# Performance work log

Hardware: AMD Instinct MI355X
Metric: run time of the kernel (lower is better)

## Reference

```python
import jax, jax.numpy as jnp
import numpy as np

INPUT_SIZE = 512
HIDDEN_SIZE = 256
B, S = 8, 2048


def setup_inputs() -> dict:
    key = jax.random.key(0)
    ks = jax.random.split(key, 9)
    d = INPUT_SIZE
    q = jax.random.normal(ks[0], (B, S, 2 * HIDDEN_SIZE), dtype=jnp.float32)
    k = jax.random.normal(ks[1], (B, S, d), dtype=jnp.float32)
    v = jax.random.normal(ks[2], (B, S, d), dtype=jnp.float32)
    # Params: module uses nn.init.normal_ (std=1); keep normal but scale for stability.
    Wq = jax.random.normal(ks[3], (2 * HIDDEN_SIZE, d), dtype=jnp.float32) * 0.02
    bq = jax.random.normal(ks[4], (d,), dtype=jnp.float32) * 0.02
    Wk = jax.random.normal(ks[5], (d, d), dtype=jnp.float32) * 0.02
    bk = jax.random.normal(ks[6], (d,), dtype=jnp.float32) * 0.02
    Wv = jax.random.normal(ks[7], (d, d), dtype=jnp.float32) * 0.02
    bv = jax.random.normal(ks[8], (d,), dtype=jnp.float32) * 0.02
    return {"q": q, "k": k, "v": v, "Wq": Wq, "bq": bq, "Wk": Wk, "bk": bk, "Wv": Wv, "bv": bv}


def reference(q, k, v, Wq, bq, Wk, bk, Wv, bv):
    d = Wq.shape[-1]
    qp = jnp.einsum('bsh,hd->bsd', q, Wq) + bq  # [B,S,d]
    kp = jnp.einsum('bse,ed->bsd', k, Wk) + bk
    vp = jnp.einsum('bse,ed->bsd', v, Wv) + bv
    scale = 1.0 / jnp.sqrt(jnp.float32(d))
    scores = jnp.einsum('bqd,bkd->bqk', qp, kp) * scale  # [B,S,S]
    attn = jax.nn.softmax(scores, axis=-1)
    return jnp.einsum('bqk,bkd->bqd', attn, vp)
```

## Files before the change

### kernel.cpp

```cpp
#include <hip/hip_runtime.h>
#include <hip/hip_bf16.h>
#include <stdint.h>


typedef __attribute__((ext_vector_type(8))) short short8;
typedef __attribute__((ext_vector_type(4))) float floatx4;

__device__ __forceinline__ unsigned short f2bf(float f) {
    union { float f; uint32_t u; } v; v.f = f;
    uint32_t u = v.u;
    return (unsigned short)((u + 0x7FFF + ((u >> 16) & 1)) >> 16);
}

#define ASYNC16(g, l)                                                          \
    __builtin_amdgcn_global_load_lds(                                          \
        (const __attribute__((address_space(1))) unsigned int*)(g),            \
        (__attribute__((address_space(3))) unsigned int*)(l), 16, 0, 0)

__global__ void wt_kernel(const float* __restrict__ Wq, const float* __restrict__ Wk,
                          const float* __restrict__ Wv, unsigned short* __restrict__ WT) {
    __shared__ float t[64][65];
    const int z = blockIdx.z;
    const float* W = (z == 0) ? Wq : ((z == 1) ? Wk : Wv);
    const int n0 = blockIdx.x * 64, k0 = blockIdx.y * 64;
    const int tx = threadIdx.x & 63, ty = threadIdx.x >> 6;
#pragma unroll
    for (int i = ty; i < 64; i += 4) t[i][tx] = W[(size_t)(k0 + i) * 512 + n0 + tx];
    __syncthreads();
#pragma unroll
    for (int i = ty; i < 64; i += 4)
        WT[(size_t)z * 262144 + (size_t)(n0 + i) * 512 + k0 + tx] = f2bf(t[tx][i]);
}

__global__ __launch_bounds__(256, 2) void proj_kernel(
    const float* __restrict__ q, const float* __restrict__ k, const float* __restrict__ v,
    const float* __restrict__ bq, const float* __restrict__ bk, const float* __restrict__ bv,
    const unsigned short* __restrict__ WT,
    unsigned short* __restrict__ qp, unsigned short* __restrict__ kp,
    unsigned short* __restrict__ vpT)
{
    __shared__ __align__(16) unsigned short At[2][64][32];
    __shared__ __align__(16) unsigned short Bt[2][512][32];

    const int z = blockIdx.z;
    const int lane = threadIdx.x & 63;
    const int wave = threadIdx.x >> 6;
    const int col = lane & 15;
    const int quad = lane >> 4;

    const float* A = (z == 0) ? q : ((z == 1) ? k : v);
    const float* bias = (z == 0) ? bq : ((z == 1) ? bk : bv);
    const unsigned short* W = WT + (size_t)z * 262144;

    const int m0 = blockIdx.x * 64;
    const int n0w = wave * 128;

    floatx4 acc[4][8];
#pragma unroll
    for (int mf = 0; mf < 4; ++mf)
#pragma unroll
        for (int nf = 0; nf < 8; ++nf) acc[mf][nf] = floatx4{0.f, 0.f, 0.f, 0.f};

    auto stageB = [&](int nb, int kc) {
#pragma unroll
        for (int jj = 0; jj < 8; ++jj) {
            const int j = wave * 8 + jj;
            const int row = j * 16 + (lane >> 2);
            const unsigned short* g =
                W + (size_t)row * 512 + kc * 32 + (((lane & 3) ^ (row & 3)) << 3);
            ASYNC16(g, &Bt[nb][j * 16][0]);
        }
    };
    auto stageA = [&](int nb, int kc) {
        const int row = wave * 16 + (lane >> 2);
        const float* ap = A + (size_t)(m0 + row) * 512 + kc * 32 + (lane & 3) * 8;
        float4 f0 = *(const float4*)ap;
        float4 f1 = *(const float4*)(ap + 4);
        short8 t;
        t[0] = f2bf(f0.x); t[1] = f2bf(f0.y); t[2] = f2bf(f0.z); t[3] = f2bf(f0.w);
        t[4] = f2bf(f1.x); t[5] = f2bf(f1.y); t[6] = f2bf(f1.z); t[7] = f2bf(f1.w);
        *(short8*)&At[nb][row][((lane & 3) ^ (row & 3)) << 3] = t;
    };

    stageB(0, 0);
    stageA(0, 0);
    for (int kc = 0; kc < 16; ++kc) {
        const int cur = kc & 1;
        __syncthreads();
        if (kc < 15) { stageB(cur ^ 1, kc + 1); stageA(cur ^ 1, kc + 1); }

        short8 a[4], bfr[8];
#pragma unroll
        for (int mf = 0; mf < 4; ++mf)
            a[mf] = *(const short8*)&At[cur][mf * 16 + col][(quad ^ (col & 3)) << 3];
#pragma unroll
        for (int nf = 0; nf < 8; ++nf)
            bfr[nf] = *(const short8*)&Bt[cur][n0w + nf * 16 + col][(quad ^ (col & 3)) << 3];
#pragma unroll
        for (int mf = 0; mf < 4; ++mf)
#pragma unroll
            for (int nf = 0; nf < 8; ++nf)
                acc[mf][nf] = __builtin_amdgcn_mfma_f32_16x16x32_bf16(a[mf], bfr[nf], acc[mf][nf], 0, 0, 0);
    }

    const float scale = (z == 0) ? 0.04419417382415922f : 1.0f;
#pragma unroll
    for (int mf = 0; mf < 4; ++mf) {
#pragma unroll
        for (int nf = 0; nf < 8; ++nf) {
            const int n = n0w + nf * 16 + col;
            const float bn2 = bias[n];
            floatx4 c = acc[mf][nf];
            if (z < 2) {
                unsigned short* outp = (z == 0) ? qp : kp;
#pragma unroll
                for (int r = 0; r < 4; ++r) {
                    int row = m0 + mf * 16 + quad * 4 + r;
                    outp[(size_t)row * 512 + n] = f2bf((c[r] + bn2) * scale);
                }
            } else {
                int row = m0 + mf * 16 + quad * 4;
                int bb = row >> 11;
                int s = row & 2047;
                ushort4 pk;
                pk.x = f2bf(c[0] + bn2); pk.y = f2bf(c[1] + bn2);
                pk.z = f2bf(c[2] + bn2); pk.w = f2bf(c[3] + bn2);
                *(ushort4*)(vpT + (((size_t)bb * 64 + (s >> 5)) * 512 + n) * 32 + (s & 31)) = pk;
            }
        }
    }
}

__global__ __launch_bounds__(512, 2) void attn_kernel(
    const unsigned short* __restrict__ qp, const unsigned short* __restrict__ kp,
    const unsigned short* __restrict__ vpT, float* __restrict__ out,
    float* __restrict__ Opart, float* __restrict__ lws)
{
    __shared__ __align__(16) unsigned short Kt[2][32][512];
    __shared__ __align__(16) unsigned short Vt[2][512][32];
    __shared__ __align__(16) unsigned short Pbuf[8][16][40];

    const int lane = threadIdx.x & 63;
    const int wave = threadIdx.x >> 6;
    const int col = lane & 15;
    const int quad = lane >> 4;
    const int b = blockIdx.x & 7;
    const int qt = (blockIdx.x >> 3) & 15;
    const int ksp = blockIdx.x >> 7;
    const int q0 = qt * 128 + wave * 16;
    const size_t rowbase = (size_t)b * 2048 + q0;

    const unsigned short* kpb = kp + (size_t)b * 2048 * 512;
    const unsigned short* vpb = vpT + ((size_t)b << 20);

    short8 aq[16];
#pragma unroll
    for (int kk = 0; kk < 16; ++kk)
        aq[kk] = *(const short8*)(qp + (rowbase + col) * 512 + kk * 32 + quad * 8);

    floatx4 o[32];
#pragma unroll
    for (int i = 0; i < 32; ++i) o[i] = floatx4{0.f, 0.f, 0.f, 0.f};
    float plsum[4] = {0.f, 0.f, 0.f, 0.f};

    auto stage = [&](int nb, int keyblk) {
#pragma unroll
        for (int j = 0; j < 4; ++j) {
            const int r = wave * 4 + j;
            const unsigned short* g =
                kpb + ((size_t)(keyblk * 32 + r) << 9) + ((lane ^ (r & 7)) << 3);
            ASYNC16(g, &Kt[nb][r][0]);
        }
        const unsigned short* vtile = vpb + ((size_t)keyblk << 14);
#pragma unroll
        for (int jj = 0; jj < 4; ++jj) {
            const int j2 = wave * 4 + jj;
            const int d = j2 * 16 + (lane >> 2);
            const unsigned short* g =
                vtile + ((size_t)d << 5) + (((lane & 3) ^ ((d >> 1) & 3)) << 3);
            ASYNC16(g, &Vt[nb][j2 * 16][0]);
        }
    };

    stage(0, ksp * 32);
    for (int kb = 0; kb < 32; ++kb) {
        const int cur = kb & 1;
        __syncthreads();
        if (kb < 31) stage(cur ^ 1, ksp * 32 + kb + 1);

        floatx4 s0 = floatx4{0.f, 0.f, 0.f, 0.f};
        floatx4 s1 = floatx4{0.f, 0.f, 0.f, 0.f};
        __builtin_amdgcn_s_setprio(1);
#pragma unroll
        for (int kk = 0; kk < 16; ++kk) {
            const int c = (kk << 2) + quad;
            short8 b0 = *(const short8*)&Kt[cur][col][(c ^ (col & 7)) << 3];
            short8 b1 = *(const short8*)&Kt[cur][16 + col][(c ^ (col & 7)) << 3];
            s0 = __builtin_amdgcn_mfma_f32_16x16x32_bf16(aq[kk], b0, s0, 0, 0, 0);
            s1 = __builtin_amdgcn_mfma_f32_16x16x32_bf16(aq[kk], b1, s1, 0, 0, 0);
        }
        __builtin_amdgcn_s_setprio(0);

#pragma unroll
        for (int r = 0; r < 4; ++r) {
            const float p0 = __expf(s0[r]);
            const float p1 = __expf(s1[r]);
            plsum[r] += p0 + p1;
            Pbuf[wave][quad * 4 + r][col]      = f2bf(p0);
            Pbuf[wave][quad * 4 + r][16 + col] = f2bf(p1);
        }
        const short8 aP = *(const short8*)&Pbuf[wave][col][quad * 8];

        __builtin_amdgcn_s_setprio(1);
#pragma unroll
        for (int nf = 0; nf < 32; ++nf) {
            const int d = nf * 16 + col;
            short8 bvf = *(const short8*)&Vt[cur][d][(quad ^ ((d >> 1) & 3)) << 3];
            o[nf] = __builtin_amdgcn_mfma_f32_16x16x32_bf16(aP, bvf, o[nf], 0, 0, 0);
        }
        __builtin_amdgcn_s_setprio(0);
    }

    float l[4];
#pragma unroll
    for (int r = 0; r < 4; ++r) {
        float acc_s = plsum[r];
#pragma unroll
        for (int off = 1; off <= 8; off <<= 1)
            acc_s += __shfl_xor(acc_s, off, 64);
        l[r] = acc_s;
    }
    float* obuf = (ksp == 0) ? out : Opart;
#pragma unroll
    for (int nf = 0; nf < 32; ++nf) {
#pragma unroll
        for (int r = 0; r < 4; ++r) {
            obuf[(rowbase + quad * 4 + r) * 512 + nf * 16 + col] = o[nf][r];
        }
    }
    if (col == 0) {
        float* lp = lws + ksp * 16384 + (int)rowbase;
#pragma unroll
        for (int r = 0; r < 4; ++r) lp[quad * 4 + r] = l[r];
    }
}

__global__ __launch_bounds__(256) void norm_kernel(float* __restrict__ out,
                                                   const float* __restrict__ Opart,
                                                   const float* __restrict__ lws)
{
    const size_t gid = (size_t)blockIdx.x * 256 + threadIdx.x;
    const int row = (int)(gid >> 7);
    const float rl = 1.0f / (lws[row] + lws[16384 + row]);
    float4 a = ((const float4*)out)[gid];
    float4 c = ((const float4*)Opart)[gid];
    float4 r;
    r.x = (a.x + c.x) * rl; r.y = (a.y + c.y) * rl;
    r.z = (a.z + c.z) * rl; r.w = (a.w + c.w) * rl;
    ((float4*)out)[gid] = r;
}

extern "C" void kernel_launch(void* const* d_in, const int* in_sizes, int n_in,
                              void* d_out, int out_size, void* d_ws, size_t ws_size,
                              hipStream_t stream) {
    const float* q  = (const float*)d_in[0];
    const float* k  = (const float*)d_in[1];
    const float* v  = (const float*)d_in[2];
    const float* Wq = (const float*)d_in[3];
    const float* bq = (const float*)d_in[4];
    const float* Wk = (const float*)d_in[5];
    const float* bk = (const float*)d_in[6];
    const float* Wv = (const float*)d_in[7];
    const float* bv = (const float*)d_in[8];
    float* out = (float*)d_out;

    unsigned short* WT  = (unsigned short*)d_ws;
    unsigned short* qp  = WT + (size_t)3 * 262144;
    unsigned short* kp  = qp + (size_t)16384 * 512;
    unsigned short* vpT = kp + (size_t)16384 * 512;
    float* Opart = (float*)(vpT + (size_t)16384 * 512);
    float* lws   = Opart + (size_t)8 * 2048 * 512;

    wt_kernel<<<dim3(8, 8, 3), 256, 0, stream>>>(Wq, Wk, Wv, WT);
    proj_kernel<<<dim3(256, 1, 3), 256, 0, stream>>>(q, k, v, bq, bk, bv, WT, qp, kp, vpT);
    attn_kernel<<<256, 512, 0, stream>>>(qp, kp, vpT, out, Opart, lws);
    norm_kernel<<<8192, 256, 0, stream>>>(out, Opart, lws);
}
```

Baseline: 323.4 us.

## Split projection N across blocks, prefetch A into registers, change LDS swizzle

The projection kernel now gives each block 256 output columns instead of 512, launched as a second grid dimension. This halves the per-wave accumulator tile and the B staging buffer so occupancy can double (launch bounds 4). The A tile's global load now goes to registers before the MFMA loop and is converted and written to LDS afterwards, overlapping load latency with compute. The LDS XOR swizzle is changed to use (row>>1)&3. The cost is that the fp32 A rows are read and converted twice, once per column half.

After: 315.1 us. -2.6%, faster.

```diff
diff --git a/kernel.cpp b/kernel.cpp
--- a/kernel.cpp
+++ b/kernel.cpp
@@ -32,7 +32,7 @@
         WT[(size_t)z * 262144 + (size_t)(n0 + i) * 512 + k0 + tx] = f2bf(t[tx][i]);
 }
 
-__global__ __launch_bounds__(256, 2) void proj_kernel(
+__global__ __launch_bounds__(256, 4) void proj_kernel(
     const float* __restrict__ q, const float* __restrict__ k, const float* __restrict__ v,
     const float* __restrict__ bq, const float* __restrict__ bk, const float* __restrict__ bv,
     const unsigned short* __restrict__ WT,
@@ -40,11 +40,12 @@
     unsigned short* __restrict__ vpT)
 {
     __shared__ __align__(16) unsigned short At[2][64][32];
-    __shared__ __align__(16) unsigned short Bt[2][512][32];
+    __shared__ __align__(16) unsigned short Bt[2][256][32];
 
     const int z = blockIdx.z;
-    const int lane = threadIdx.x & 63;
-    const int wave = threadIdx.x >> 6;
+    const int tid = threadIdx.x;
+    const int lane = tid & 63;
+    const int wave = tid >> 6;
     const int col = lane & 15;
     const int quad = lane >> 4;
 
@@ -53,62 +54,69 @@
     const unsigned short* W = WT + (size_t)z * 262144;
 
     const int m0 = blockIdx.x * 64;
-    const int n0w = wave * 128;
-
-    floatx4 acc[4][8];
+    const int n0b = blockIdx.y * 256;
+
+    floatx4 acc[4][4];
 #pragma unroll
     for (int mf = 0; mf < 4; ++mf)
 #pragma unroll
-        for (int nf = 0; nf < 8; ++nf) acc[mf][nf] = floatx4{0.f, 0.f, 0.f, 0.f};
+        for (int nf = 0; nf < 4; ++nf) acc[mf][nf] = floatx4{0.f, 0.f, 0.f, 0.f};
 
     auto stageB = [&](int nb, int kc) {
 #pragma unroll
-        for (int jj = 0; jj < 8; ++jj) {
-            const int j = wave * 8 + jj;
-            const int row = j * 16 + (lane >> 2);
+        for (int j = 0; j < 4; ++j) {
+            const int rr = (wave * 4 + j) * 16 + (lane >> 2);
             const unsigned short* g =
-                W + (size_t)row * 512 + kc * 32 + (((lane & 3) ^ (row & 3)) << 3);
-            ASYNC16(g, &Bt[nb][j * 16][0]);
-        }
-    };
-    auto stageA = [&](int nb, int kc) {
-        const int row = wave * 16 + (lane >> 2);
-        const float* ap = A + (size_t)(m0 + row) * 512 + kc * 32 + (lane & 3) * 8;
-        float4 f0 = *(const float4*)ap;
-        float4 f1 = *(const float4*)(ap + 4);
+                W + (size_t)(n0b + rr) * 512 + kc * 32 + (((lane & 3) ^ ((rr >> 1) & 3)) << 3);
+            ASYNC16(g, &Bt[nb][(wave * 4 + j) * 16][0]);
+        }
+    };
+
+    float4 fA0, fA1;
+    const int arow = tid >> 2;
+    auto loadA = [&](int kc) {
+        const float* ap = A + (size_t)(m0 + arow) * 512 + kc * 32 + (tid & 3) * 8;
+        fA0 = *(const float4*)ap;
+        fA1 = *(const float4*)(ap + 4);
+    };
+    auto writeA = [&](int nb) {
         short8 t;
-        t[0] = f2bf(f0.x); t[1] = f2bf(f0.y); t[2] = f2bf(f0.z); t[3] = f2bf(f0.w);
-        t[4] = f2bf(f1.x); t[5] = f2bf(f1.y); t[6] = f2bf(f1.z); t[7] = f2bf(f1.w);
-        *(short8*)&At[nb][row][((lane & 3) ^ (row & 3)) << 3] = t;
+        t[0] = f2bf(fA0.x); t[1] = f2bf(fA0.y); t[2] = f2bf(fA0.z); t[3] = f2bf(fA0.w);
+        t[4] = f2bf(fA1.x); t[5] = f2bf(fA1.y); t[6] = f2bf(fA1.z); t[7] = f2bf(fA1.w);
+        *(short8*)&At[nb][arow][(((tid & 3) ^ ((arow >> 1) & 3)) << 3)] = t;
     };
 
     stageB(0, 0);
-    stageA(0, 0);
+    loadA(0);
+    writeA(0);
     for (int kc = 0; kc < 16; ++kc) {
         const int cur = kc & 1;
         __syncthreads();
-        if (kc < 15) { stageB(cur ^ 1, kc + 1); stageA(cur ^ 1, kc + 1); }
-
-        short8 a[4], bfr[8];
+        if (kc < 15) { stageB(cur ^ 1, kc + 1); loadA(kc + 1); }
+
+        const int rsw = (quad ^ ((col >> 1) & 3)) << 3;
+        short8 a[4], bfr[4];
 #pragma unroll
         for (int mf = 0; mf < 4; ++mf)
-            a[mf] = *(const short8*)&At[cur][mf * 16 + col][(quad ^ (col & 3)) << 3];
-#pragma unroll
-        for (int nf = 0; nf < 8; ++nf)
-            bfr[nf] = *(const short8*)&Bt[cur][n0w + nf * 16 + col][(quad ^ (col & 3)) << 3];
+            a[mf] = *(const short8*)&At[cur][mf * 16 + col][rsw];
+#pragma unroll
+        for (int nf = 0; nf < 4; ++nf)
+            bfr[nf] = *(const short8*)&Bt[cur][wave * 64 + nf * 16 + col][rsw];
 #pragma unroll
         for (int mf = 0; mf < 4; ++mf)
 #pragma unroll
-            for (int nf = 0; nf < 8; ++nf)
+            for (int nf = 0; nf < 4; ++nf)
                 acc[mf][nf] = __builtin_amdgcn_mfma_f32_16x16x32_bf16(a[mf], bfr[nf], acc[mf][nf], 0, 0, 0);
+
+        if (kc < 15) writeA(cur ^ 1);
     }
 
     const float scale = (z == 0) ? 0.04419417382415922f : 1.0f;
 #pragma unroll
     for (int mf = 0; mf < 4; ++mf) {
 #pragma unroll
-        for (int nf = 0; nf < 8; ++nf) {
-            const int n = n0w + nf * 16 + col;
+        for (int nf = 0; nf < 4; ++nf) {
+            const int n = n0b + wave * 64 + nf * 16 + col;
             const float bn2 = bias[n];
             floatx4 c = acc[mf][nf];
             if (z < 2) {
@@ -282,7 +290,7 @@
     float* lws   = Opart + (size_t)8 * 2048 * 512;
 
     wt_kernel<<<dim3(8, 8, 3), 256, 0, stream>>>(Wq, Wk, Wv, WT);
-    proj_kernel<<<dim3(256, 1, 3), 256, 0, stream>>>(q, k, v, bq, bk, bv, WT, qp, kp, vpT);
+    proj_kernel<<<dim3(256, 2, 3), 256, 0, stream>>>(q, k, v, bq, bk, bv, WT, qp, kp, vpT);
     attn_kernel<<<256, 512, 0, stream>>>(qp, kp, vpT, out, Opart, lws);
     norm_kernel<<<8192, 256, 0, stream>>>(out, Opart, lws);
 }
```
